# Optimization experiments

Measured on AMD Instinct MI355X. Metric: run time of the kernel, lower is better.

## Reference

```python
import jax, jax.numpy as jnp
import numpy as np

N = 100000      # nodes
E = 1_600_000   # edges (avg degree 16)
IN, HID, OUT = 128, 128, 64


def _prep(edge_index, n):
    """Add self-loops and compute symmetric GCN normalization per edge."""
    loops = jnp.arange(n, dtype=edge_index.dtype)
    src = jnp.concatenate([edge_index[0], loops])  # [E+N]
    dst = jnp.concatenate([edge_index[1], loops])  # [E+N]
    deg = jax.ops.segment_sum(jnp.ones(src.shape, jnp.float32), dst, num_segments=n)
    dinv = jnp.where(deg > 0, jax.lax.rsqrt(deg), 0.0)
    norm = dinv[src] * dinv[dst]                   # [E+N]
    return src, dst, norm


def gcn_conv(x, src, dst, norm, W, b, n):
    # PyG GCNConv: transform first, then normalized gather/scatter-add aggregate
    h = x @ W                                      # [N, C_out]
    msg = h[src] * norm[:, None]                   # [E+N, C_out] irregular gather
    return jax.ops.segment_sum(msg, dst, num_segments=n) + b


def setup_inputs() -> dict:
    key = jax.random.key(0)
    k1, k2, k3, k4 = jax.random.split(key, 4)
    x = jax.random.normal(k1, (N, IN), dtype=jnp.float32)
    edge_index = jax.random.randint(k2, (2, E), 0, N, dtype=jnp.int32)
    W1 = jax.random.normal(k3, (IN, HID), dtype=jnp.float32) * (1.0 / np.sqrt(IN))
    b1 = jnp.zeros((HID,), jnp.float32)
    W2 = jax.random.normal(k4, (HID, OUT), dtype=jnp.float32) * (1.0 / np.sqrt(HID))
    b2 = jnp.zeros((OUT,), jnp.float32)
    return {"x": x, "W1": W1, "b1": b1, "W2": W2, "b2": b2, "edge_index": edge_index}


def reference(x, W1, b1, W2, b2, edge_index):
    n = x.shape[0]
    src, dst, norm = _prep(edge_index, n)
    h = gcn_conv(x, src, dst, norm, W1, b1, n)
    h = jax.nn.softmax(h, axis=1)
    return gcn_conv(h, src, dst, norm, W2, b2, n)
```

## Files before the change

### kernel.cpp

```cpp
#include <hip/hip_runtime.h>
#include <hip/hip_fp16.h>
#include <cstdint>
#include <cstddef>


#define BSHIFT 8
#define NBPAD 512
#define NWG 256
#define CAP 6144

typedef _Float16 half8 __attribute__((ext_vector_type(8)));
typedef float f32x4 __attribute__((ext_vector_type(4)));

__device__ __forceinline__ void h8_to_f(const uint4& u, float* f) {
  const __half2* hp = (const __half2*)&u;
#pragma unroll
  for (int i = 0; i < 4; ++i) {
    float2 t = __half22float2(hp[i]);
    f[2 * i] = t.x;
    f[2 * i + 1] = t.y;
  }
}

__device__ __forceinline__ void fma8(float* acc, float w, const float* v) {
#pragma unroll
  for (int i = 0; i < 8; ++i) acc[i] = fmaf(w, v[i], acc[i]);
}

__device__ __forceinline__ int block_scan256(int v, int* wsums) {
  const int lane = threadIdx.x & 63;
  const int wid = threadIdx.x >> 6;
  int x = v;
#pragma unroll
  for (int d = 1; d < 64; d <<= 1) {
    int y = __shfl_up(x, d);
    if (lane >= d) x += y;
  }
  if (lane == 63) wsums[wid] = x;
  __syncthreads();
  int off = 0;
#pragma unroll
  for (int j = 0; j < 4; ++j)
    if (j < wid) off += wsums[j];
  return off + x;
}

__global__ __launch_bounds__(256) void wg_count(const int* __restrict__ dst,
                                                int* __restrict__ counts,
                                                int E, int nb, int slice) {
  __shared__ int lh[NBPAD];
  const int w = blockIdx.x;
  for (int i = threadIdx.x; i < nb; i += 256) lh[i] = 0;
  __syncthreads();
  const int e0 = w * slice;
  const int e1 = min(e0 + slice, E);
  for (int e = e0 + threadIdx.x; e < e1; e += 256)
    atomicAdd(&lh[dst[e] >> BSHIFT], 1);
  __syncthreads();
  for (int i = threadIdx.x; i < nb; i += 256) counts[(size_t)w * NBPAD + i] = lh[i];
}

__global__ __launch_bounds__(1024) void scan_buckets(const int* __restrict__ counts,
                                                     int* __restrict__ bstart,
                                                     int* __restrict__ row_start,
                                                     int nb, int n, int E) {
  __shared__ int wsum[16];
  const int tid = threadIdx.x;
  const int lane = tid & 63;
  const int wid = tid >> 6;
  int v = 0;
  if (tid < nb) {
#pragma unroll 4
    for (int i = 0; i < NWG; ++i) v += counts[(size_t)i * NBPAD + tid];
  }
  int x = v;
#pragma unroll
  for (int d = 1; d < 64; d <<= 1) {
    int y = __shfl_up(x, d);
    if (lane >= d) x += y;
  }
  if (lane == 63) wsum[wid] = x;
  __syncthreads();
  if (wid == 0) {
    int w = (lane < 16) ? wsum[lane] : 0;
#pragma unroll
    for (int d = 1; d < 16; d <<= 1) {
      int y = __shfl_up(w, d);
      if (lane >= d) w += y;
    }
    if (lane < 16) wsum[lane] = w;
  }
  __syncthreads();
  int boff = (wid > 0) ? wsum[wid - 1] : 0;
  int incl = boff + x;
  if (tid < nb) {
    bstart[tid] = incl - v;
    if (tid == nb - 1) bstart[nb] = incl;
  }
  if (tid == 0) row_start[n] = E;
}

__global__ __launch_bounds__(256) void cell_scan(const int* __restrict__ counts,
                                                 const int* __restrict__ bstart,
                                                 int* __restrict__ cur, int nb) {
  __shared__ int wsums[4];
  const int b = blockIdx.x;
  const int tid = threadIdx.x;
  int v = counts[(size_t)tid * NBPAD + b];
  int incl = block_scan256(v, wsums);
  cur[(size_t)tid * NBPAD + b] = bstart[b] + incl - v;
}

__global__ __launch_bounds__(256) void wg_scatter(const int* __restrict__ src,
                                                  const int* __restrict__ dst,
                                                  const int* __restrict__ cur,
                                                  unsigned* __restrict__ staging,
                                                  int E, int nb, int slice) {
  __shared__ int lc[NBPAD];
  const int w = blockIdx.x;
  for (int i = threadIdx.x; i < nb; i += 256) lc[i] = cur[(size_t)w * NBPAD + i];
  __syncthreads();
  const int e0 = w * slice;
  const int e1 = min(e0 + slice, E);
  for (int e = e0 + threadIdx.x; e < e1; e += 256) {
    int d = dst[e];
    int p = atomicAdd(&lc[d >> BSHIFT], 1);
    staging[p] = ((unsigned)(d & 255) << 24) | (unsigned)src[e];
  }
}

__global__ __launch_bounds__(256) void bucket_finalize(const unsigned* __restrict__ staging,
                                                       const int* __restrict__ bstart,
                                                       int* __restrict__ csr_src,
                                                       int* __restrict__ row_start,
                                                       float* __restrict__ dinv, int n) {
  __shared__ int lcnt[256];
  __shared__ int lcur[256];
  __shared__ int wsums[4];
  __shared__ int lbuf[CAP];
  const int b = blockIdx.x;
  const int tid = threadIdx.x;
  const int n0 = b << BSHIFT;
  const int s0 = bstart[b];
  const int cnt = bstart[b + 1] - s0;

  lcnt[tid] = 0;
  __syncthreads();
  for (int i = tid; i < cnt; i += 256)
    atomicAdd(&lcnt[staging[s0 + i] >> 24], 1);
  __syncthreads();

  const int v = lcnt[tid];
  const int incl = block_scan256(v, wsums);
  const int excl = incl - v;
  lcur[tid] = excl;
  const int node = n0 + tid;
  if (node < n) {
    row_start[node] = s0 + excl;
    dinv[node] = rsqrtf((float)v + 1.0f);
  }
  __syncthreads();

  for (int i = tid; i < cnt; i += 256) {
    unsigned p = staging[s0 + i];
    int pos = atomicAdd(&lcur[p >> 24], 1);
    int s = (int)(p & 0xFFFFFFu);
    if (pos < CAP) lbuf[pos] = s;
    else csr_src[s0 + pos] = s;
  }
  __syncthreads();
  const int lim = cnt < CAP ? cnt : CAP;
  for (int i = tid; i < lim; i += 256) csr_src[s0 + i] = lbuf[i];
}

__global__ __launch_bounds__(256) void make_pack(const int* __restrict__ csr_src,
                                                 const float* __restrict__ dinv,
                                                 int2* __restrict__ pack, int E) {
  int e = blockIdx.x * 256 + threadIdx.x;
  if (e < E) {
    int s = csr_src[e];
    pack[e] = make_int2(s, __float_as_int(dinv[s]));
  }
}

template <int M>
__global__ __launch_bounds__(256) void pack_w(const float* __restrict__ W,
                                              _Float16* __restrict__ Wp) {
  int e = blockIdx.x * 256 + threadIdx.x;
  if (e < 128 * M) {
    int k = e / M, c = e % M;
    int t = k >> 5, g = (k >> 3) & 3, j = k & 7;
    Wp[(((size_t)t * M + c) * 4 + g) * 8 + j] = (_Float16)W[e];
  }
}

template <int M, bool HIN>
__global__ __launch_bounds__(256) void gemm_mfma(const void* __restrict__ Xp,
                                                 const _Float16* __restrict__ Wp,
                                                 _Float16* __restrict__ H, int N) {
  constexpr int CT = M / 16;
  const int wave = threadIdx.x >> 6;
  const int lane = threadIdx.x & 63;
  const int row0 = (blockIdx.x * 4 + wave) * 16;
  if (row0 >= N) return;
  const int r = lane & 15;
  const int g = lane >> 4;
  int row = row0 + r;
  if (row >= N) row = N - 1;

  f32x4 acc[CT];
#pragma unroll
  for (int c = 0; c < CT; ++c) acc[c] = (f32x4){0.f, 0.f, 0.f, 0.f};

#pragma unroll
  for (int t = 0; t < 4; ++t) {
    half8 a;
    if constexpr (HIN) {
      a = *(const half8*)((const _Float16*)Xp + (size_t)row * 128 + t * 32 + g * 8);
    } else {
      const float* xp = (const float*)Xp + (size_t)row * 128 + t * 32 + g * 8;
      float4 x0 = *(const float4*)xp;
      float4 x1 = *(const float4*)(xp + 4);
      a[0] = (_Float16)x0.x; a[1] = (_Float16)x0.y;
      a[2] = (_Float16)x0.z; a[3] = (_Float16)x0.w;
      a[4] = (_Float16)x1.x; a[5] = (_Float16)x1.y;
      a[6] = (_Float16)x1.z; a[7] = (_Float16)x1.w;
    }
#pragma unroll
    for (int c = 0; c < CT; ++c) {
      half8 b = *(const half8*)(Wp + (((size_t)t * M + c * 16 + r) * 4 + g) * 8);
      acc[c] = __builtin_amdgcn_mfma_f32_16x16x32_f16(a, b, acc[c], 0, 0, 0);
    }
  }

#pragma unroll
  for (int c = 0; c < CT; ++c) {
#pragma unroll
    for (int i = 0; i < 4; ++i) {
      int rr = row0 + 4 * g + i;
      if (rr < N) H[(size_t)rr * M + c * 16 + r] = (_Float16)acc[c][i];
    }
  }
}

template <int LPG>
__device__ __forceinline__ void edge1(const uint4* __restrict__ hv,
                                      const int2* __restrict__ pack,
                                      int e, int lane, float* acc) {
  int2 p = pack[e];
  uint4 r = hv[(size_t)p.x * LPG + lane];
  float v[8];
  h8_to_f(r, v);
  fma8(acc, __int_as_float(p.y), v);
}

template <int F, bool SM, bool OUTHALF>
__global__ __launch_bounds__(256) void aggregate(const __half* __restrict__ h,
                                                 const int* __restrict__ row_start,
                                                 const int2* __restrict__ pack,
                                                 const float* __restrict__ dinv,
                                                 const float* __restrict__ bias,
                                                 void* __restrict__ out, int n) {
  constexpr int LPG = F / 8;
  constexpr int GPB = 256 / LPG;
  const int node = blockIdx.x * GPB + (int)(threadIdx.x / LPG);
  const int lane = threadIdx.x % LPG;
  if (node >= n) return;

  const uint4* hv = (const uint4*)h;
  const float di = dinv[node];

  float acc[8];
  {
    uint4 su = hv[(size_t)node * LPG + lane];
    float sf[8];
    h8_to_f(su, sf);
#pragma unroll
    for (int i = 0; i < 8; ++i) acc[i] = di * sf[i];
  }

  int e = row_start[node];
  const int e1 = row_start[node + 1];

  int2 p[4];
  if (e + 4 <= e1) {
#pragma unroll
    for (int j = 0; j < 4; ++j) p[j] = pack[e + j];
  }
  while (e + 8 <= e1) {
    uint4 r[4];
#pragma unroll
    for (int j = 0; j < 4; ++j) r[j] = hv[(size_t)p[j].x * LPG + lane];
    int2 pn[4];
#pragma unroll
    for (int j = 0; j < 4; ++j) pn[j] = pack[e + 4 + j];
#pragma unroll
    for (int j = 0; j < 4; ++j) {
      float v[8];
      h8_to_f(r[j], v);
      fma8(acc, __int_as_float(p[j].y), v);
    }
#pragma unroll
    for (int j = 0; j < 4; ++j) p[j] = pn[j];
    e += 4;
  }
  if (e + 4 <= e1) {
    uint4 r[4];
#pragma unroll
    for (int j = 0; j < 4; ++j) r[j] = hv[(size_t)p[j].x * LPG + lane];
#pragma unroll
    for (int j = 0; j < 4; ++j) {
      float v[8];
      h8_to_f(r[j], v);
      fma8(acc, __int_as_float(p[j].y), v);
    }
    e += 4;
  }
  for (; e < e1; ++e) edge1<LPG>(hv, pack, e, lane, acc);

  {
    const float4* bv = (const float4*)bias;
    float4 b0 = bv[lane * 2], b1 = bv[lane * 2 + 1];
    acc[0] = fmaf(di, acc[0], b0.x);
    acc[1] = fmaf(di, acc[1], b0.y);
    acc[2] = fmaf(di, acc[2], b0.z);
    acc[3] = fmaf(di, acc[3], b0.w);
    acc[4] = fmaf(di, acc[4], b1.x);
    acc[5] = fmaf(di, acc[5], b1.y);
    acc[6] = fmaf(di, acc[6], b1.z);
    acc[7] = fmaf(di, acc[7], b1.w);
  }

  if constexpr (SM) {
    float m = acc[0];
#pragma unroll
    for (int i = 1; i < 8; ++i) m = fmaxf(m, acc[i]);
#pragma unroll
    for (int off = LPG / 2; off >= 1; off >>= 1) m = fmaxf(m, __shfl_xor(m, off));
    float ex[8], ssum = 0.f;
#pragma unroll
    for (int i = 0; i < 8; ++i) {
      ex[i] = __expf(acc[i] - m);
      ssum += ex[i];
    }
#pragma unroll
    for (int off = LPG / 2; off >= 1; off >>= 1) ssum += __shfl_xor(ssum, off);
    float r = 1.0f / ssum;
#pragma unroll
    for (int i = 0; i < 8; ++i) acc[i] = ex[i] * r;
  }

  if constexpr (OUTHALF) {
    union { __half2 h2[4]; uint4 u; } cv;
#pragma unroll
    for (int i = 0; i < 4; ++i)
      cv.h2[i] = __floats2half2_rn(acc[2 * i], acc[2 * i + 1]);
    ((uint4*)out)[(size_t)node * LPG + lane] = cv.u;
  } else {
    float4* ov = (float4*)out;
    ov[(size_t)node * (F / 4) + lane * 2] =
        make_float4(acc[0], acc[1], acc[2], acc[3]);
    ov[(size_t)node * (F / 4) + lane * 2 + 1] =
        make_float4(acc[4], acc[5], acc[6], acc[7]);
  }
}

extern "C" void kernel_launch(void* const* d_in, const int* in_sizes, int n_in,
                              void* d_out, int out_size, void* d_ws, size_t ws_size,
                              hipStream_t stream) {
  const float* x  = (const float*)d_in[0];
  const float* W1 = (const float*)d_in[1];
  const float* b1 = (const float*)d_in[2];
  const float* W2 = (const float*)d_in[3];
  const float* b2 = (const float*)d_in[4];
  const int*   ei = (const int*)d_in[5];

  const int N = in_sizes[0] / 128;
  const int E = in_sizes[5] / 2;
  const int NB = (N + 255) >> BSHIFT;
  const int SLICE = (E + NWG - 1) / NWG;
  const int* srcp = ei;
  const int* dstp = ei + E;

  auto align256 = [](size_t v) { return (v + 255) & ~(size_t)255; };
  char* ws = (char*)d_ws;
  size_t o_dinv   = 0;
  size_t o_rs     = align256(o_dinv + (size_t)N * 4);
  size_t o_cnts   = align256(o_rs + (size_t)(N + 1) * 4);
  size_t o_cur    = align256(o_cnts + (size_t)NWG * NBPAD * 4);
  size_t o_bstart = align256(o_cur + (size_t)NWG * NBPAD * 4);
  size_t o_wp1    = align256(o_bstart + (size_t)(NBPAD + 1) * 4);
  size_t o_wp2    = align256(o_wp1 + (size_t)128 * 128 * 2);
  size_t o_stg    = align256(o_wp2 + (size_t)128 * 64 * 2);
  size_t o_csr    = align256(o_stg + (size_t)E * 4);
  size_t o_pack   = align256(o_csr + (size_t)E * 4);
  size_t o_h1     = align256(o_pack + (size_t)E * 8);
  size_t o_s      = align256(o_h1 + (size_t)N * 128 * 2);

  float*    dinv     = (float*)(ws + o_dinv);
  int*      rowstart = (int*)(ws + o_rs);
  int*      counts   = (int*)(ws + o_cnts);
  int*      cur      = (int*)(ws + o_cur);
  int*      bstart   = (int*)(ws + o_bstart);
  _Float16* wp1      = (_Float16*)(ws + o_wp1);
  _Float16* wp2      = (_Float16*)(ws + o_wp2);
  unsigned* staging  = (unsigned*)(ws + o_stg);
  int*      csr_src  = (int*)(ws + o_csr);
  int2*     pack     = (int2*)(ws + o_pack);
  _Float16* h1       = (_Float16*)(ws + o_h1);
  _Float16* sbuf     = (_Float16*)(ws + o_s);

  wg_count<<<NWG, 256, 0, stream>>>(dstp, counts, E, NB, SLICE);
  scan_buckets<<<1, 1024, 0, stream>>>(counts, bstart, rowstart, NB, N, E);
  cell_scan<<<NB, 256, 0, stream>>>(counts, bstart, cur, NB);
  wg_scatter<<<NWG, 256, 0, stream>>>(srcp, dstp, cur, staging, E, NB, SLICE);
  bucket_finalize<<<NB, 256, 0, stream>>>(staging, bstart, csr_src, rowstart, dinv, N);
  make_pack<<<(E + 255) / 256, 256, 0, stream>>>(csr_src, dinv, pack, E);

  pack_w<128><<<(128 * 128 + 255) / 256, 256, 0, stream>>>(W1, wp1);
  pack_w<64><<<(128 * 64 + 255) / 256, 256, 0, stream>>>(W2, wp2);

  gemm_mfma<128, false><<<(N + 63) / 64, 256, 0, stream>>>(x, wp1, h1, N);
  aggregate<128, true, true><<<(N + 15) / 16, 256, 0, stream>>>(
      (const __half*)h1, rowstart, pack, dinv, b1, sbuf, N);
  gemm_mfma<64, true><<<(N + 63) / 64, 256, 0, stream>>>(sbuf, wp2, h1, N);
  aggregate<64, false, false><<<(N + 31) / 32, 256, 0, stream>>>(
      (const __half*)h1, rowstart, pack, dinv, b2, d_out, N);
}
```

Measured before the change: 206.5 us.

## Fuse pack creation into bucket finalize and simplify aggregate edge loop

Splits bucket_finalize into a histogram kernel that writes row_start and dinv and a second kernel that writes the (src, dinv[src]) pack array directly. This removes the csr_src intermediate buffer and the separate make_pack pass. The aggregate edge loop is also rewritten as a single prefetching loop over 4-edge batches, where missing tail edges are clamped to a valid index and given zero weight, replacing the scalar tail loop. The extra pass re-reads staging, and the padded tail batches issue redundant gathers.

```diff
diff --git a/kernel.cpp b/kernel.cpp
--- a/kernel.cpp
+++ b/kernel.cpp
@@ -129,14 +129,39 @@
   }
 }
 
-__global__ __launch_bounds__(256) void bucket_finalize(const unsigned* __restrict__ staging,
-                                                       const int* __restrict__ bstart,
-                                                       int* __restrict__ csr_src,
-                                                       int* __restrict__ row_start,
-                                                       float* __restrict__ dinv, int n) {
+__global__ __launch_bounds__(256) void bucket_hist(const unsigned* __restrict__ staging,
+                                                   const int* __restrict__ bstart,
+                                                   int* __restrict__ row_start,
+                                                   float* __restrict__ dinv, int n) {
   __shared__ int lcnt[256];
+  __shared__ int wsums[4];
+  const int b = blockIdx.x;
+  const int tid = threadIdx.x;
+  const int n0 = b << BSHIFT;
+  const int s0 = bstart[b];
+  const int cnt = bstart[b + 1] - s0;
+
+  lcnt[tid] = 0;
+  __syncthreads();
+  for (int i = tid; i < cnt; i += 256)
+    atomicAdd(&lcnt[staging[s0 + i] >> 24], 1);
+  __syncthreads();
+
+  const int v = lcnt[tid];
+  const int incl = block_scan256(v, wsums);
+  const int node = n0 + tid;
+  if (node < n) {
+    row_start[node] = s0 + incl - v;
+    dinv[node] = rsqrtf((float)v + 1.0f);
+  }
+}
+
+__global__ __launch_bounds__(256) void bucket_pack(const unsigned* __restrict__ staging,
+                                                   const int* __restrict__ bstart,
+                                                   const int* __restrict__ row_start,
+                                                   const float* __restrict__ dinv,
+                                                   int2* __restrict__ pack, int n) {
   __shared__ int lcur[256];
-  __shared__ int wsums[4];
   __shared__ int lbuf[CAP];
   const int b = blockIdx.x;
   const int tid = threadIdx.x;
@@ -144,21 +169,8 @@
   const int s0 = bstart[b];
   const int cnt = bstart[b + 1] - s0;
 
-  lcnt[tid] = 0;
-  __syncthreads();
-  for (int i = tid; i < cnt; i += 256)
-    atomicAdd(&lcnt[staging[s0 + i] >> 24], 1);
-  __syncthreads();
-
-  const int v = lcnt[tid];
-  const int incl = block_scan256(v, wsums);
-  const int excl = incl - v;
-  lcur[tid] = excl;
   const int node = n0 + tid;
-  if (node < n) {
-    row_start[node] = s0 + excl;
-    dinv[node] = rsqrtf((float)v + 1.0f);
-  }
+  lcur[tid] = (node < n) ? (row_start[node] - s0) : 0;
   __syncthreads();
 
   for (int i = tid; i < cnt; i += 256) {
@@ -166,20 +178,13 @@
     int pos = atomicAdd(&lcur[p >> 24], 1);
     int s = (int)(p & 0xFFFFFFu);
     if (pos < CAP) lbuf[pos] = s;
-    else csr_src[s0 + pos] = s;
+    else pack[s0 + pos] = make_int2(s, __float_as_int(dinv[s]));
   }
   __syncthreads();
   const int lim = cnt < CAP ? cnt : CAP;
-  for (int i = tid; i < lim; i += 256) csr_src[s0 + i] = lbuf[i];
-}
-
-__global__ __launch_bounds__(256) void make_pack(const int* __restrict__ csr_src,
-                                                 const float* __restrict__ dinv,
-                                                 int2* __restrict__ pack, int E) {
-  int e = blockIdx.x * 256 + threadIdx.x;
-  if (e < E) {
-    int s = csr_src[e];
-    pack[e] = make_int2(s, __float_as_int(dinv[s]));
+  for (int i = tid; i < lim; i += 256) {
+    int s = lbuf[i];
+    pack[s0 + i] = make_int2(s, __float_as_int(dinv[s]));
   }
 }
 
@@ -243,15 +248,15 @@
   }
 }
 
-template <int LPG>
-__device__ __forceinline__ void edge1(const uint4* __restrict__ hv,
-                                      const int2* __restrict__ pack,
-                                      int e, int lane, float* acc) {
-  int2 p = pack[e];
-  uint4 r = hv[(size_t)p.x * LPG + lane];
-  float v[8];
-  h8_to_f(r, v);
-  fma8(acc, __int_as_float(p.y), v);
+__device__ __forceinline__ void pack_batch(const int2* __restrict__ pack,
+                                           int e, int e1, int2* p) {
+#pragma unroll
+  for (int j = 0; j < 4; ++j) {
+    int idx = e + j;
+    bool ok = idx < e1;
+    p[j] = pack[ok ? idx : (e1 - 1)];
+    if (!ok) p[j].y = 0;
+  }
 }
 
 template <int F, bool SM, bool OUTHALF>
@@ -279,44 +284,32 @@
     for (int i = 0; i < 8; ++i) acc[i] = di * sf[i];
   }
 
-  int e = row_start[node];
+  const int e0 = row_start[node];
   const int e1 = row_start[node + 1];
-
-  int2 p[4];
-  if (e + 4 <= e1) {
-#pragma unroll
-    for (int j = 0; j < 4; ++j) p[j] = pack[e + j];
-  }
-  while (e + 8 <= e1) {
-    uint4 r[4];
-#pragma unroll
-    for (int j = 0; j < 4; ++j) r[j] = hv[(size_t)p[j].x * LPG + lane];
-    int2 pn[4];
-#pragma unroll
-    for (int j = 0; j < 4; ++j) pn[j] = pack[e + 4 + j];
-#pragma unroll
-    for (int j = 0; j < 4; ++j) {
-      float v[8];
-      h8_to_f(r[j], v);
-      fma8(acc, __int_as_float(p[j].y), v);
-    }
-#pragma unroll
-    for (int j = 0; j < 4; ++j) p[j] = pn[j];
-    e += 4;
-  }
-  if (e + 4 <= e1) {
-    uint4 r[4];
-#pragma unroll
-    for (int j = 0; j < 4; ++j) r[j] = hv[(size_t)p[j].x * LPG + lane];
-#pragma unroll
-    for (int j = 0; j < 4; ++j) {
-      float v[8];
-      h8_to_f(r[j], v);
-      fma8(acc, __int_as_float(p[j].y), v);
-    }
-    e += 4;
-  }
-  for (; e < e1; ++e) edge1<LPG>(hv, pack, e, lane, acc);
+  if (e0 < e1) {
+    int2 p[4];
+    pack_batch(pack, e0, e1, p);
+    int e = e0;
+    for (;;) {
+      uint4 r[4];
+#pragma unroll
+      for (int j = 0; j < 4; ++j) r[j] = hv[(size_t)p[j].x * LPG + lane];
+      const int en = e + 4;
+      const bool more = en < e1;
+      int2 pn[4];
+      if (more) pack_batch(pack, en, e1, pn);
+#pragma unroll
+      for (int j = 0; j < 4; ++j) {
+        float v[8];
+        h8_to_f(r[j], v);
+        fma8(acc, __int_as_float(p[j].y), v);
+      }
+      if (!more) break;
+#pragma unroll
+      for (int j = 0; j < 4; ++j) p[j] = pn[j];
+      e = en;
+    }
+  }
 
   {
     const float4* bv = (const float4*)bias;
@@ -392,8 +385,7 @@
   size_t o_wp1    = align256(o_bstart + (size_t)(NBPAD + 1) * 4);
   size_t o_wp2    = align256(o_wp1 + (size_t)128 * 128 * 2);
   size_t o_stg    = align256(o_wp2 + (size_t)128 * 64 * 2);
-  size_t o_csr    = align256(o_stg + (size_t)E * 4);
-  size_t o_pack   = align256(o_csr + (size_t)E * 4);
+  size_t o_pack   = align256(o_stg + (size_t)E * 4);
   size_t o_h1     = align256(o_pack + (size_t)E * 8);
   size_t o_s      = align256(o_h1 + (size_t)N * 128 * 2);
 
@@ -405,7 +397,6 @@
   _Float16* wp1      = (_Float16*)(ws + o_wp1);
   _Float16* wp2      = (_Float16*)(ws + o_wp2);
   unsigned* staging  = (unsigned*)(ws + o_stg);
-  int*      csr_src  = (int*)(ws + o_csr);
   int2*     pack     = (int2*)(ws + o_pack);
   _Float16* h1       = (_Float16*)(ws + o_h1);
   _Float16* sbuf     = (_Float16*)(ws + o_s);
@@ -414,8 +405,8 @@
   scan_buckets<<<1, 1024, 0, stream>>>(counts, bstart, rowstart, NB, N, E);
   cell_scan<<<NB, 256, 0, stream>>>(counts, bstart, cur, NB);
   wg_scatter<<<NWG, 256, 0, stream>>>(srcp, dstp, cur, staging, E, NB, SLICE);
-  bucket_finalize<<<NB, 256, 0, stream>>>(staging, bstart, csr_src, rowstart, dinv, N);
-  make_pack<<<(E + 255) / 256, 256, 0, stream>>>(csr_src, dinv, pack, E);
+  bucket_hist<<<NB, 256, 0, stream>>>(staging, bstart, rowstart, dinv, N);
+  bucket_pack<<<NB, 256, 0, stream>>>(staging, bstart, rowstart, dinv, pack, N);
 
   pack_w<128><<<(128 * 128 + 255) / 256, 256, 0, stream>>>(W1, wp1);
   pack_w<64><<<(128 * 64 + 255) / 256, 256, 0, stream>>>(W2, wp2);
```

Result: no change. 202.7 us (-1.8%).
